# Kernel optimization log

Measured on AMD Instinct MI355X. Metric: run time of the kernel, lower is better.

The kernel has to match this reference:

```python
import jax, jax.numpy as jnp
import numpy as np

N, E, D_IN, HID, D_OUT, MAX_DEG = 30000, 480000, 128, 128, 128, 48


def setup_inputs() -> dict:
    key = jax.random.key(0)
    ks = jax.random.split(key, 8)
    input_matrix = jax.random.normal(ks[0], (N, D_IN), jnp.float32)
    edge_src_idxs = jnp.sort(jax.random.randint(ks[1], (E,), 0, N))
    edge_trg_idxs = jax.random.randint(ks[2], (E,), 0, N)
    s = 1.0 / np.sqrt(HID)  # pytorch LSTM init bound
    W_ih = jax.random.uniform(ks[3], (4 * HID, D_IN), jnp.float32, -s, s)
    W_hh = jax.random.uniform(ks[4], (4 * HID, HID), jnp.float32, -s, s)
    b_ih = jax.random.uniform(ks[5], (4 * HID,), jnp.float32, -s, s)
    b_hh = jax.random.uniform(ks[6], (4 * HID,), jnp.float32, -s, s)
    xb = np.sqrt(6.0 / (D_IN + HID + D_OUT))  # xavier uniform
    W_out = jax.random.uniform(ks[7], (D_IN + HID, D_OUT), jnp.float32, -xb, xb)
    return {
        "input_matrix": input_matrix,
        "W_ih": W_ih, "W_hh": W_hh, "b_ih": b_ih, "b_hh": b_hh,
        "W_out": W_out,
        "edge_src_idxs": edge_src_idxs,
        "edge_trg_idxs": edge_trg_idxs,
        "max_deg": MAX_DEG,
    }


def _lstm_last(dense, mask, W_ih, W_hh, b):
    # dense: [N, T, d], mask: [N, T] -> final hidden state at last valid step, [N, H]
    H = W_hh.shape[1]

    def step(carry, xs):
        h, c = carry
        x_t, m_t = xs  # [N, d], [N]
        gates = x_t @ W_ih.T + h @ W_hh.T + b  # [N, 4H], pytorch gate order i,f,g,o
        i, f, g, o = jnp.split(gates, 4, axis=-1)
        c2 = jax.nn.sigmoid(f) * c + jax.nn.sigmoid(i) * jnp.tanh(g)
        h2 = jax.nn.sigmoid(o) * jnp.tanh(c2)
        m = m_t[:, None]
        return (jnp.where(m, h2, h), jnp.where(m, c2, c)), None

    h0 = jnp.zeros((dense.shape[0], H), dense.dtype)
    (h, _), _ = jax.lax.scan(step, (h0, h0), (dense.transpose(1, 0, 2), mask.T))
    return h


def reference(input_matrix, W_ih, W_hh, b_ih, b_hh, W_out,
              edge_src_idxs, edge_trg_idxs, max_deg):
    n, d = input_matrix.shape
    e = edge_src_idxs.shape[0]
    neighbors = input_matrix[edge_trg_idxs]  # [E, d] gather
    # edge_src_idxs is sorted: position of each edge within its source group
    counts = jax.ops.segment_sum(jnp.ones((e,), jnp.int32), edge_src_idxs,
                                 num_segments=n)
    starts = jnp.cumsum(counts) - counts  # exclusive cumsum
    pos = jnp.arange(e) - starts[edge_src_idxs]  # [E]
    # pad ragged neighbor sequences into [N, max_deg, d] (overflow dropped)
    dense = jnp.zeros((n, max_deg, d), input_matrix.dtype).at[edge_src_idxs, pos].set(neighbors)
    mask = jnp.zeros((n, max_deg), bool).at[edge_src_idxs, pos].set(True)
    agg = _lstm_last(dense, mask, W_ih, W_hh, b_ih + b_hh)  # [N, H]; zeros for isolated nodes
    return jnp.concatenate([input_matrix, agg], axis=1) @ W_out
```

## Files before the change

kernel.cpp:

```cpp
#include <hip/hip_runtime.h>

#define NN 30000
#define NE 480000
#define NG 512
#define MAXD 48
#define BATCH 32
#define NB 938
#define HPAD 144
#define NGB 469

typedef __attribute__((ext_vector_type(8))) short short8;
typedef __attribute__((ext_vector_type(4))) short s16x4;
typedef __attribute__((ext_vector_type(4))) float f32x4;

static __device__ __forceinline__ short f2bs(float f) {
  unsigned u = __builtin_bit_cast(unsigned, f);
  u = (u + 0x7fffu + ((u >> 16) & 1u)) >> 16;
  return (short)u;
}
static __device__ __forceinline__ float bs2f(short s) {
  unsigned u = ((unsigned)(unsigned short)s) << 16;
  return __builtin_bit_cast(float, u);
}
static __device__ __forceinline__ float sigf(float x) {
  return __builtin_amdgcn_rcpf(1.0f + __expf(-x));
}
static __device__ __forceinline__ float tanh_(float x) {
  return 1.0f - 2.0f * __builtin_amdgcn_rcpf(1.0f + __expf(2.0f * x));
}
static __device__ __forceinline__ void gl_lds16(const short* g, short* l) {
  __builtin_amdgcn_global_load_lds(
      (const __attribute__((address_space(1))) void*)g,
      (__attribute__((address_space(3))) void*)l, 16, 0, 0);
}

#define PIN_AGPR(w_) asm("" : "+a"(w_))

#define EDGE_BLKS 1875
__global__ void k_edges_wcvt(const int* __restrict__ src, int* __restrict__ starts,
                             int* __restrict__ ends,
                             const float* __restrict__ W_ih,
                             const float* __restrict__ W_hh,
                             const float* __restrict__ Wout,
                             short* __restrict__ wih_s, short* __restrict__ whh_s,
                             short* __restrict__ wout_s) {
  const int b = blockIdx.x, tid = threadIdx.x;
  if (b < EDGE_BLKS) {
    int e = b * 256 + tid;
    if (e >= NE) return;
    int s = src[e];
    if (e == 0 || src[e - 1] != s) starts[s] = e;
    if (e == NE - 1 || src[e + 1] != s) ends[s] = e + 1;
    return;
  }
  const int f = b - EDGE_BLKS;
  const int wv = tid >> 6, lq = (tid >> 4) & 3, lc = tid & 15;
  if (f < 64) {
    const float* W = (f < 32) ? W_ih : W_hh;
    short* dst = (f < 32) ? wih_s : whh_s;
    const int ff = f & 31;
    const int g = ff >> 3, db = (ff >> 2) & 1, kt = ff & 3;
    const float* p = &W[(g * 128 + wv * 32 + db * 16 + lc) * 128 + kt * 32 + lq * 8];
    f32x4 a = *(const f32x4*)p;
    f32x4 c = *(const f32x4*)(p + 4);
    short8 w;
    w[0] = f2bs(a[0]); w[1] = f2bs(a[1]); w[2] = f2bs(a[2]); w[3] = f2bs(a[3]);
    w[4] = f2bs(c[0]); w[5] = f2bs(c[1]); w[6] = f2bs(c[2]); w[7] = f2bs(c[3]);
    *(short8*)&dst[(ff * 256 + tid) * 8] = w;
  } else {
    const int fo = f - 64;
    const int db = fo >> 3, kt = fo & 7;
    short8 w;
#pragma unroll
    for (int jj = 0; jj < 8; ++jj)
      w[jj] = f2bs(Wout[(kt * 32 + lq * 8 + jj) * 128 + wv * 32 + db * 16 + lc]);
    *(short8*)&wout_s[(fo * 256 + tid) * 8] = w;
  }
}

__global__ void k_hist(const int* __restrict__ starts, const int* __restrict__ ends,
                       int* __restrict__ ghist) {
  __shared__ int h[MAXD + 1];
  const int tid = threadIdx.x;
  if (tid <= MAXD) h[tid] = 0;
  __syncthreads();
  int n = blockIdx.x * 256 + tid;
  if (n < NN) {
    int c = ends[n] - starts[n]; c = c > MAXD ? MAXD : c;
    atomicAdd(&h[c], 1);
  }
  __syncthreads();
  if (tid <= MAXD && h[tid] > 0) atomicAdd(&ghist[tid], h[tid]);
}

__global__ void k_scan(const int* __restrict__ ghist, int* __restrict__ gbase) {
  __shared__ int h[MAXD + 1];
  const int tid = threadIdx.x;
  if (tid <= MAXD) h[tid] = ghist[tid];
  __syncthreads();
  if (tid == 0) {
    int tot = 0;
    for (int b = MAXD; b >= 0; --b) { int c = h[b]; h[b] = tot; tot += c; }
  }
  __syncthreads();
  if (tid <= MAXD) gbase[tid] = h[tid];
}

__global__ void k_scat2(const int* __restrict__ starts, const int* __restrict__ ends,
                        int* __restrict__ gbase, int* __restrict__ order) {
  __shared__ int lh[MAXD + 1];
  __shared__ int lbase[MAXD + 1];
  const int tid = threadIdx.x;
  if (tid <= MAXD) lh[tid] = 0;
  __syncthreads();
  int n = blockIdx.x * 256 + tid;
  int c = 0, rank = 0;
  if (n < NN) {
    c = ends[n] - starts[n]; c = c > MAXD ? MAXD : c;
    rank = atomicAdd(&lh[c], 1);
  }
  __syncthreads();
  if (tid <= MAXD && lh[tid] > 0) lbase[tid] = atomicAdd(&gbase[tid], lh[tid]);
  __syncthreads();
  if (n < NN) order[lbase[c] + rank] = n;
}

__global__ void k_nbr(const int* __restrict__ src, const int* __restrict__ trg,
                      const int* __restrict__ starts, int* __restrict__ nbr) {
  int e = blockIdx.x * 256 + threadIdx.x;
  if (e >= NE) return;
  int s = src[e];
  int pos = e - starts[s];
  if (pos < MAXD) nbr[s * MAXD + pos] = trg[e];
}

__global__ __launch_bounds__(256)
__attribute__((amdgpu_waves_per_eu(2, 2))) void k_proj(
    const float* __restrict__ x, const short* __restrict__ wih_s,
    const float* __restrict__ b_ih, const float* __restrict__ b_hh,
    short* __restrict__ proj) {
  __shared__ __align__(16) short xs[64 * HPAD];
  const int tid = threadIdx.x;
  const int wv = tid >> 6, lane = tid & 63, lq = lane >> 4, lc = lane & 15;
  const int base = blockIdx.x * 64;

  for (int idx4 = tid; idx4 < 64 * 32; idx4 += 256) {
    int row = idx4 >> 5, k4 = (idx4 & 31) << 2;
    f32x4 v = (f32x4){0.f, 0.f, 0.f, 0.f};
    if (base + row < NN) v = *(const f32x4*)&x[(base + row) * 128 + k4];
    s16x4 p; p[0] = f2bs(v[0]); p[1] = f2bs(v[1]); p[2] = f2bs(v[2]); p[3] = f2bs(v[3]);
    *(s16x4*)&xs[row * HPAD + k4] = p;
  }
  const short8* wihv = (const short8*)wih_s;
  short8 wfrag[4][2][4];
#pragma unroll
  for (int g = 0; g < 4; ++g)
#pragma unroll
    for (int db = 0; db < 2; ++db)
#pragma unroll
      for (int kt = 0; kt < 4; ++kt) {
        short8 w = wihv[(g * 8 + db * 4 + kt) * 256 + tid];
        PIN_AGPR(w);
        wfrag[g][db][kt] = w;
      }
  float bias_v[4][2];
#pragma unroll
  for (int g = 0; g < 4; ++g)
#pragma unroll
    for (int db = 0; db < 2; ++db) {
      int j = g * 128 + wv * 32 + db * 16 + lc;
      bias_v[g][db] = b_ih[j] + b_hh[j];
    }
  __syncthreads();

#pragma unroll
  for (int mt = 0; mt < 4; ++mt) {
    short8 afrag[4];
#pragma unroll
    for (int kt = 0; kt < 4; ++kt)
      afrag[kt] = *(const short8*)&xs[(mt * 16 + lc) * HPAD + kt * 32 + lq * 8];
    f32x4 acc[4][2];
#pragma unroll
    for (int g = 0; g < 4; ++g)
#pragma unroll
      for (int db = 0; db < 2; ++db) {
        float b = bias_v[g][db];
        acc[g][db] = (f32x4){b, b, b, b};
#pragma unroll
        for (int kt = 0; kt < 4; ++kt)
          acc[g][db] = __builtin_amdgcn_mfma_f32_16x16x32_bf16(
              afrag[kt], wfrag[g][db][kt], acc[g][db], 0, 0, 0);
      }
#pragma unroll
    for (int r = 0; r < 4; ++r) {
      int row = base + mt * 16 + lq * 4 + r;
      if (row < NN) {
        short8 w;
        w[0] = f2bs(acc[0][0][r]); w[1] = f2bs(acc[0][1][r]);
        w[2] = f2bs(acc[1][0][r]); w[3] = f2bs(acc[1][1][r]);
        w[4] = f2bs(acc[2][0][r]); w[5] = f2bs(acc[2][1][r]);
        w[6] = f2bs(acc[3][0][r]); w[7] = f2bs(acc[3][1][r]);
        *(short8*)&proj[row * NG + (wv * 16 + lc) * 8] = w;
      }
    }
  }
}

__global__ __launch_bounds__(256)
__attribute__((amdgpu_waves_per_eu(2, 2))) void k_lstm(
    const short* __restrict__ whh_s, const short* __restrict__ proj,
    const int* __restrict__ order, const int* __restrict__ starts,
    const int* __restrict__ ends, const int* __restrict__ nbr,
    short* __restrict__ agg) {
  __shared__ __align__(16) short h_s[2][BATCH * HPAD];
  __shared__ __align__(16) short pbuf[4][8][64 * 8];
  __shared__ unsigned short nbr_s[BATCH][MAXD];
  __shared__ int nodes_s[BATCH];
  __shared__ int cnts_s[BATCH];

  const int tid = threadIdx.x;
  const int wv = tid >> 6, lane = tid & 63, lq = lane >> 4, lc = lane & 15;

  const short8* whhv = (const short8*)whh_s;
  short8 wfrag[4][2][4];
#pragma unroll
  for (int g = 0; g < 4; ++g)
#pragma unroll
    for (int db = 0; db < 2; ++db)
#pragma unroll
      for (int kt = 0; kt < 4; ++kt) {
        short8 w = whhv[(g * 8 + db * 4 + kt) * 256 + tid];
        PIN_AGPR(w);
        wfrag[g][db][kt] = w;
      }

  const int batch = blockIdx.x;
  if (tid < BATCH) {
    int gidx = batch * BATCH + tid;
    int node = 0, c = 0;
    if (gidx < NN) {
      node = order[gidx];
      c = ends[node] - starts[node]; c = c > MAXD ? MAXD : c;
    }
    nodes_s[tid] = node;
    cnts_s[tid] = c;
  }
  __syncthreads();
  for (int idx = tid; idx < BATCH * HPAD / 2; idx += 256)
    ((int*)h_s[0])[idx] = 0;
  for (int idx = tid; idx < BATCH * MAXD; idx += 256) {
    int m = idx / MAXD, p = idx - m * MAXD;
    nbr_s[m][p] = (unsigned short)nbr[nodes_s[m] * MAXD + p];
  }
  __syncthreads();
  const int T = cnts_s[0];

  int cp[2];
#pragma unroll
  for (int mt = 0; mt < 2; ++mt) {
    int p = 0;
#pragma unroll
    for (int r = 0; r < 4; ++r) p |= cnts_s[mt * 16 + lq * 4 + r] << (r * 8);
    cp[mt] = p;
  }

  float c_v[2][2][4];
  s16x4 hvp[2][2];
#pragma unroll
  for (int mt = 0; mt < 2; ++mt)
#pragma unroll
    for (int db = 0; db < 2; ++db) {
#pragma unroll
      for (int r = 0; r < 4; ++r) c_v[mt][db][r] = 0.0f;
      hvp[mt][db] = (s16x4){0, 0, 0, 0};
    }

  const int pcol = (wv * 16 + lc) * 8;
  if (T > 0) {
#pragma unroll
    for (int mt = 0; mt < 2; ++mt)
#pragma unroll
      for (int r = 0; r < 4; ++r) {
        int m = mt * 16 + lq * 4 + r;
        int nb_i = (0 < ((cp[mt] >> (r * 8)) & 255)) ? (int)nbr_s[m][0] : 0;
        gl_lds16(&proj[nb_i * NG + pcol], &pbuf[wv][mt * 4 + r][0]);
      }
  }

  for (int t = 0; t < T; ++t) {
    __syncthreads();
    const short* hb = h_s[t & 1];
    short* hw = h_s[(t + 1) & 1];
    const int tn = t + 1;
    const int ts = tn < MAXD ? tn : 0;
#pragma unroll
    for (int mt = 0; mt < 2; ++mt) {
      short8 pv[4];
#pragma unroll
      for (int r = 0; r < 4; ++r)
        pv[r] = *(const short8*)&pbuf[wv][mt * 4 + r][lane * 8];
      f32x4 acc[4][2];
#pragma unroll
      for (int g = 0; g < 4; ++g)
#pragma unroll
        for (int db = 0; db < 2; ++db)
#pragma unroll
          for (int r = 0; r < 4; ++r)
            acc[g][db][r] = bs2f(pv[r][g * 2 + db]);
      __builtin_amdgcn_sched_barrier(0);
      if (tn < T) {
#pragma unroll
        for (int r = 0; r < 4; ++r) {
          int m = mt * 16 + lq * 4 + r;
          int nb_i = (tn < ((cp[mt] >> (r * 8)) & 255)) ? (int)nbr_s[m][ts] : 0;
          gl_lds16(&proj[nb_i * NG + pcol], &pbuf[wv][mt * 4 + r][0]);
        }
      }
      __builtin_amdgcn_sched_barrier(0);
      short8 afrag[4];
#pragma unroll
      for (int kt = 0; kt < 4; ++kt)
        afrag[kt] = *(const short8*)&hb[(mt * 16 + lc) * HPAD + kt * 32 + lq * 8];
#pragma unroll
      for (int g = 0; g < 4; ++g)
#pragma unroll
        for (int db = 0; db < 2; ++db)
#pragma unroll
          for (int kt = 0; kt < 4; ++kt)
            acc[g][db] = __builtin_amdgcn_mfma_f32_16x16x32_bf16(
                afrag[kt], wfrag[g][db][kt], acc[g][db], 0, 0, 0);
#pragma unroll
      for (int db = 0; db < 2; ++db)
#pragma unroll
        for (int r = 0; r < 4; ++r) {
          float iv = sigf(acc[0][db][r]);
          float fv = sigf(acc[1][db][r]);
          float gv = tanh_(acc[2][db][r]);
          float ov = sigf(acc[3][db][r]);
          float c2 = fv * c_v[mt][db][r] + iv * gv;
          float h2 = ov * tanh_(c2);
          if (t < ((cp[mt] >> (r * 8)) & 255)) {
            c_v[mt][db][r] = c2;
            hvp[mt][db][r] = f2bs(h2);
          }
        }
#pragma unroll
      for (int db = 0; db < 2; ++db)
#pragma unroll
        for (int r = 0; r < 4; ++r)
          hw[(mt * 16 + lq * 4 + r) * HPAD + wv * 32 + db * 16 + lc] =
              hvp[mt][db][r];
    }
  }
  __syncthreads();
  const short* hf = h_s[T & 1];
  for (int idx = tid; idx < BATCH * 128; idx += 256) {
    int m = idx >> 7, d = idx & 127;
    if (batch * BATCH + m < NN) agg[nodes_s[m] * 128 + d] = hf[m * HPAD + d];
  }
}

__global__ __launch_bounds__(256, 2) void k_out(
    const float* __restrict__ x, const short* __restrict__ agg,
    const short* __restrict__ wout_s, float* __restrict__ out) {
  __shared__ __align__(16) short xs[64 * 272];
  const int tid = threadIdx.x;
  const int wv = tid >> 6, lane = tid & 63, lq = lane >> 4, lc = lane & 15;
  const int base = blockIdx.x * 64;

  for (int idx4 = tid; idx4 < 64 * 32; idx4 += 256) {
    int row = idx4 >> 5, k4 = (idx4 & 31) << 2;
    f32x4 v = (f32x4){0.f, 0.f, 0.f, 0.f};
    if (base + row < NN) v = *(const f32x4*)&x[(base + row) * 128 + k4];
    s16x4 p; p[0] = f2bs(v[0]); p[1] = f2bs(v[1]); p[2] = f2bs(v[2]); p[3] = f2bs(v[3]);
    *(s16x4*)&xs[row * 272 + k4] = p;
    s16x4 a = (s16x4){0, 0, 0, 0};
    if (base + row < NN) a = *(const s16x4*)&agg[(base + row) * 128 + k4];
    *(s16x4*)&xs[row * 272 + 128 + k4] = a;
  }
  const short8* wov = (const short8*)wout_s;
  short8 wf[2][8];
#pragma unroll
  for (int db = 0; db < 2; ++db)
#pragma unroll
    for (int kt = 0; kt < 8; ++kt)
      wf[db][kt] = wov[(db * 8 + kt) * 256 + tid];
  __syncthreads();

#pragma unroll
  for (int mt = 0; mt < 4; ++mt) {
    short8 afrag[8];
#pragma unroll
    for (int kt = 0; kt < 8; ++kt)
      afrag[kt] = *(const short8*)&xs[(mt * 16 + lc) * 272 + kt * 32 + lq * 8];
    f32x4 acc[2];
#pragma unroll
    for (int db = 0; db < 2; ++db) {
      acc[db] = (f32x4){0.f, 0.f, 0.f, 0.f};
#pragma unroll
      for (int kt = 0; kt < 8; ++kt)
        acc[db] = __builtin_amdgcn_mfma_f32_16x16x32_bf16(
            afrag[kt], wf[db][kt], acc[db], 0, 0, 0);
    }
#pragma unroll
    for (int db = 0; db < 2; ++db)
#pragma unroll
      for (int r = 0; r < 4; ++r) {
        int row = base + mt * 16 + lq * 4 + r;
        if (row < NN)
          out[row * 128 + wv * 32 + db * 16 + lc] = acc[db][r];
      }
  }
}

extern "C" void kernel_launch(void* const* d_in, const int* in_sizes, int n_in,
                              void* d_out, int out_size, void* d_ws,
                              size_t ws_size, hipStream_t stream) {
  (void)in_sizes; (void)n_in; (void)out_size; (void)ws_size;
  const float* x     = (const float*)d_in[0];
  const float* W_ih  = (const float*)d_in[1];
  const float* W_hh  = (const float*)d_in[2];
  const float* b_ih  = (const float*)d_in[3];
  const float* b_hh  = (const float*)d_in[4];
  const float* W_out = (const float*)d_in[5];
  const int*   esrc  = (const int*)d_in[6];
  const int*   etrg  = (const int*)d_in[7];
  float* out = (float*)d_out;
  char* ws = (char*)d_ws;

  int*   starts = (int*)(ws + 0);
  int*   ends   = (int*)(ws + 120064);
  int*   ghist  = (int*)(ws + 240128);
  int*   order  = (int*)(ws + 240384);
  int*   nbr    = (int*)(ws + 360448);
  short* proj   = (short*)(ws + 6382848);
  short* agg    = (short*)(ws + 37102848);
  short* wih_s  = (short*)(ws + 44782848);
  short* whh_s  = (short*)(ws + 44913920);
  short* wout_s = (short*)(ws + 45045760);
  int*   gbase  = (int*)(ws + 45111296);

  (void)hipMemsetAsync(d_ws, 0, 240384, stream);

  k_edges_wcvt<<<EDGE_BLKS + 80, 256, 0, stream>>>(esrc, starts, ends, W_ih,
                                                   W_hh, W_out, wih_s, whh_s,
                                                   wout_s);
  k_hist <<<118, 256, 0, stream>>>(starts, ends, ghist);
  k_scan <<<1, 64, 0, stream>>>(ghist, gbase);
  k_scat2<<<118, 256, 0, stream>>>(starts, ends, gbase, order);
  k_nbr  <<<1875, 256, 0, stream>>>(esrc, etrg, starts, nbr);
  k_proj <<<NGB, 256, 0, stream>>>(x, wih_s, b_ih, b_hh, proj);
  k_lstm <<<NB, 256, 0, stream>>>(whh_s, proj, order, starts, ends, nbr, agg);
  k_out  <<<NGB, 256, 0, stream>>>(x, agg, wout_s, out);
}
```

Baseline: 260.1 us.

## Prescale gate weights by log2e, fuse preprocessing kernels, streamline LSTM activations

```diff
diff --git a/kernel.cpp b/kernel.cpp
--- a/kernel.cpp
+++ b/kernel.cpp
@@ -12,21 +12,15 @@
 typedef __attribute__((ext_vector_type(8))) short short8;
 typedef __attribute__((ext_vector_type(4))) short s16x4;
 typedef __attribute__((ext_vector_type(4))) float f32x4;
+typedef __attribute__((ext_vector_type(4))) int i32x4;
+
+#define L2E 1.44269504089f
+#define L2E2 2.88539008178f
 
 static __device__ __forceinline__ short f2bs(float f) {
   unsigned u = __builtin_bit_cast(unsigned, f);
   u = (u + 0x7fffu + ((u >> 16) & 1u)) >> 16;
   return (short)u;
-}
-static __device__ __forceinline__ float bs2f(short s) {
-  unsigned u = ((unsigned)(unsigned short)s) << 16;
-  return __builtin_bit_cast(float, u);
-}
-static __device__ __forceinline__ float sigf(float x) {
-  return __builtin_amdgcn_rcpf(1.0f + __expf(-x));
-}
-static __device__ __forceinline__ float tanh_(float x) {
-  return 1.0f - 2.0f * __builtin_amdgcn_rcpf(1.0f + __expf(2.0f * x));
 }
 static __device__ __forceinline__ void gl_lds16(const short* g, short* l) {
   __builtin_amdgcn_global_load_lds(
@@ -60,12 +54,13 @@
     short* dst = (f < 32) ? wih_s : whh_s;
     const int ff = f & 31;
     const int g = ff >> 3, db = (ff >> 2) & 1, kt = ff & 3;
+    const float s = (g == 2) ? L2E2 : L2E;
     const float* p = &W[(g * 128 + wv * 32 + db * 16 + lc) * 128 + kt * 32 + lq * 8];
     f32x4 a = *(const f32x4*)p;
     f32x4 c = *(const f32x4*)(p + 4);
     short8 w;
-    w[0] = f2bs(a[0]); w[1] = f2bs(a[1]); w[2] = f2bs(a[2]); w[3] = f2bs(a[3]);
-    w[4] = f2bs(c[0]); w[5] = f2bs(c[1]); w[6] = f2bs(c[2]); w[7] = f2bs(c[3]);
+    w[0] = f2bs(a[0] * s); w[1] = f2bs(a[1] * s); w[2] = f2bs(a[2] * s); w[3] = f2bs(a[3] * s);
+    w[4] = f2bs(c[0] * s); w[5] = f2bs(c[1] * s); w[6] = f2bs(c[2] * s); w[7] = f2bs(c[3] * s);
     *(short8*)&dst[(ff * 256 + tid) * 8] = w;
   } else {
     const int fo = f - 64;
@@ -78,38 +73,33 @@
   }
 }
 
-__global__ void k_hist(const int* __restrict__ starts, const int* __restrict__ ends,
-                       int* __restrict__ ghist) {
+__global__ void k_nbr_hist(const int* __restrict__ src, const int* __restrict__ trg,
+                           const int* __restrict__ starts, const int* __restrict__ ends,
+                           int* __restrict__ nbr, int* __restrict__ ghist) {
   __shared__ int h[MAXD + 1];
   const int tid = threadIdx.x;
   if (tid <= MAXD) h[tid] = 0;
   __syncthreads();
-  int n = blockIdx.x * 256 + tid;
-  if (n < NN) {
-    int c = ends[n] - starts[n]; c = c > MAXD ? MAXD : c;
+  int e = blockIdx.x * 256 + tid;
+  if (e < NE) {
+    int s = src[e];
+    int pos = e - starts[s];
+    if (pos < MAXD) nbr[s * MAXD + pos] = trg[e];
+  }
+  if (e < NN) {
+    int c = ends[e] - starts[e]; c = c > MAXD ? MAXD : c;
     atomicAdd(&h[c], 1);
   }
   __syncthreads();
   if (tid <= MAXD && h[tid] > 0) atomicAdd(&ghist[tid], h[tid]);
 }
 
-__global__ void k_scan(const int* __restrict__ ghist, int* __restrict__ gbase) {
-  __shared__ int h[MAXD + 1];
-  const int tid = threadIdx.x;
-  if (tid <= MAXD) h[tid] = ghist[tid];
-  __syncthreads();
-  if (tid == 0) {
-    int tot = 0;
-    for (int b = MAXD; b >= 0; --b) { int c = h[b]; h[b] = tot; tot += c; }
-  }
-  __syncthreads();
-  if (tid <= MAXD) gbase[tid] = h[tid];
-}
-
 __global__ void k_scat2(const int* __restrict__ starts, const int* __restrict__ ends,
-                        int* __restrict__ gbase, int* __restrict__ order) {
+                        const int* __restrict__ ghist, int* __restrict__ gclaim,
+                        int* __restrict__ order) {
   __shared__ int lh[MAXD + 1];
   __shared__ int lbase[MAXD + 1];
+  __shared__ int sbase[MAXD + 1];
   const int tid = threadIdx.x;
   if (tid <= MAXD) lh[tid] = 0;
   __syncthreads();
@@ -119,19 +109,15 @@
     c = ends[n] - starts[n]; c = c > MAXD ? MAXD : c;
     rank = atomicAdd(&lh[c], 1);
   }
-  __syncthreads();
-  if (tid <= MAXD && lh[tid] > 0) lbase[tid] = atomicAdd(&gbase[tid], lh[tid]);
+  if (tid == 0) {
+    int tot = 0;
+    for (int b = MAXD; b >= 0; --b) { sbase[b] = tot; tot += ghist[b]; }
+  }
+  __syncthreads();
+  if (tid <= MAXD && lh[tid] > 0)
+    lbase[tid] = sbase[tid] + atomicAdd(&gclaim[tid], lh[tid]);
   __syncthreads();
   if (n < NN) order[lbase[c] + rank] = n;
-}
-
-__global__ void k_nbr(const int* __restrict__ src, const int* __restrict__ trg,
-                      const int* __restrict__ starts, int* __restrict__ nbr) {
-  int e = blockIdx.x * 256 + threadIdx.x;
-  if (e >= NE) return;
-  int s = src[e];
-  int pos = e - starts[s];
-  if (pos < MAXD) nbr[s * MAXD + pos] = trg[e];
 }
 
 __global__ __launch_bounds__(256)
@@ -169,7 +155,7 @@
 #pragma unroll
     for (int db = 0; db < 2; ++db) {
       int j = g * 128 + wv * 32 + db * 16 + lc;
-      bias_v[g][db] = b_ih[j] + b_hh[j];
+      bias_v[g][db] = (b_ih[j] + b_hh[j]) * ((g == 2) ? L2E2 : L2E);
     }
   __syncthreads();
 
@@ -295,18 +281,19 @@
     const int ts = tn < MAXD ? tn : 0;
 #pragma unroll
     for (int mt = 0; mt < 2; ++mt) {
-      short8 pv[4];
+      i32x4 pvi[4];
 #pragma unroll
       for (int r = 0; r < 4; ++r)
-        pv[r] = *(const short8*)&pbuf[wv][mt * 4 + r][lane * 8];
+        pvi[r] = *(const i32x4*)&pbuf[wv][mt * 4 + r][lane * 8];
       f32x4 acc[4][2];
 #pragma unroll
       for (int g = 0; g < 4; ++g)
 #pragma unroll
-        for (int db = 0; db < 2; ++db)
-#pragma unroll
-          for (int r = 0; r < 4; ++r)
-            acc[g][db][r] = bs2f(pv[r][g * 2 + db]);
+        for (int r = 0; r < 4; ++r) {
+          unsigned u = (unsigned)pvi[r][g];
+          acc[g][0][r] = __builtin_bit_cast(float, u << 16);
+          acc[g][1][r] = __builtin_bit_cast(float, u & 0xffff0000u);
+        }
       __builtin_amdgcn_sched_barrier(0);
       if (tn < T) {
 #pragma unroll
@@ -333,12 +320,17 @@
       for (int db = 0; db < 2; ++db)
 #pragma unroll
         for (int r = 0; r < 4; ++r) {
-          float iv = sigf(acc[0][db][r]);
-          float fv = sigf(acc[1][db][r]);
-          float gv = tanh_(acc[2][db][r]);
-          float ov = sigf(acc[3][db][r]);
-          float c2 = fv * c_v[mt][db][r] + iv * gv;
-          float h2 = ov * tanh_(c2);
+          float Ei = __builtin_amdgcn_exp2f(-acc[0][db][r]);
+          float Eg = __builtin_amdgcn_exp2f(fminf(acc[2][db][r], 125.f));
+          float ig = (Eg - 1.f) *
+                     __builtin_amdgcn_rcpf((1.f + Ei) * (1.f + Eg));
+          float fv = __builtin_amdgcn_rcpf(
+              1.f + __builtin_amdgcn_exp2f(-acc[1][db][r]));
+          float c2 = fv * c_v[mt][db][r] + ig;
+          float Eo = __builtin_amdgcn_exp2f(-acc[3][db][r]);
+          float Ec = __builtin_amdgcn_exp2f(fminf(c2 * L2E2, 125.f));
+          float h2 = (Ec - 1.f) *
+                     __builtin_amdgcn_rcpf((1.f + Eo) * (1.f + Ec));
           if (t < ((cp[mt] >> (r * 8)) & 255)) {
             c_v[mt][db][r] = c2;
             hvp[mt][db][r] = f2bs(h2);
@@ -431,24 +423,22 @@
   int*   starts = (int*)(ws + 0);
   int*   ends   = (int*)(ws + 120064);
   int*   ghist  = (int*)(ws + 240128);
-  int*   order  = (int*)(ws + 240384);
-  int*   nbr    = (int*)(ws + 360448);
-  short* proj   = (short*)(ws + 6382848);
-  short* agg    = (short*)(ws + 37102848);
-  short* wih_s  = (short*)(ws + 44782848);
-  short* whh_s  = (short*)(ws + 44913920);
-  short* wout_s = (short*)(ws + 45045760);
-  int*   gbase  = (int*)(ws + 45111296);
-
-  (void)hipMemsetAsync(d_ws, 0, 240384, stream);
+  int*   gclaim = (int*)(ws + 240384);
+  int*   order  = (int*)(ws + 240640);
+  int*   nbr    = (int*)(ws + 360704);
+  short* proj   = (short*)(ws + 6120704);
+  short* agg    = (short*)(ws + 36840704);
+  short* wih_s  = (short*)(ws + 44520704);
+  short* whh_s  = (short*)(ws + 44651776);
+  short* wout_s = (short*)(ws + 44782848);
+
+  (void)hipMemsetAsync(d_ws, 0, 240640, stream);
 
   k_edges_wcvt<<<EDGE_BLKS + 80, 256, 0, stream>>>(esrc, starts, ends, W_ih,
                                                    W_hh, W_out, wih_s, whh_s,
                                                    wout_s);
-  k_hist <<<118, 256, 0, stream>>>(starts, ends, ghist);
-  k_scan <<<1, 64, 0, stream>>>(ghist, gbase);
-  k_scat2<<<118, 256, 0, stream>>>(starts, ends, gbase, order);
-  k_nbr  <<<1875, 256, 0, stream>>>(esrc, etrg, starts, nbr);
+  k_nbr_hist<<<1875, 256, 0, stream>>>(esrc, etrg, starts, ends, nbr, ghist);
+  k_scat2<<<118, 256, 0, stream>>>(starts, ends, ghist, gclaim, order);
   k_proj <<<NGB, 256, 0, stream>>>(x, wih_s, b_ih, b_hh, proj);
   k_lstm <<<NB, 256, 0, stream>>>(whh_s, proj, order, starts, ends, nbr, agg);
   k_out  <<<NGB, 256, 0, stream>>>(x, agg, wout_s, out);
```

After: 250.0 us. -3.9%, faster.
